# Performance work log

Hardware: AMD Instinct MI355X
Metric: run time of the kernel (lower is better)

Reference implementation:

```python
import jax, jax.numpy as jnp
import numpy as np

N, CIN, MID, OUT, H, W = 8, 512, 256, 256, 56, 56
HY, WY = 28, 28
EPS = 1e-5
K = 9  # 3x3 kernel points


def setup_inputs() -> dict:
    key = jax.random.key(0)
    ks = jax.random.split(key, 16)
    d = {}
    d["x"] = jax.random.normal(ks[0], (N, CIN, H, W), jnp.float32)
    d["y"] = jax.random.normal(ks[1], (N, MID, HY, WY), jnp.float32)
    d["conv1_w"] = jax.random.normal(ks[2], (MID, CIN), jnp.float32) * 0.02
    d["bn1_gamma"] = jax.random.uniform(ks[3], (MID,), jnp.float32) + 0.5
    d["bn1_beta"] = jax.random.normal(ks[4], (MID,), jnp.float32) * 0.1
    d["bn1_mean"] = jax.random.normal(ks[5], (MID,), jnp.float32) * 0.1
    d["bn1_var"] = jax.random.uniform(ks[6], (MID,), jnp.float32) + 0.5
    d["att_w"] = jax.random.normal(ks[7], (2, 2 * MID), jnp.float32) * 0.02
    d["att_b"] = jax.random.normal(ks[8], (2,), jnp.float32) * 0.1
    d["off_w"] = jax.random.normal(ks[9], (2 * K, MID, 3, 3), jnp.float32) * 0.01
    d["dcn_w"] = jax.random.normal(ks[10], (OUT, MID, 3, 3), jnp.float32) * 0.02
    d["bn2_gamma"] = jax.random.uniform(ks[11], (OUT,), jnp.float32) + 0.5
    d["bn2_beta"] = jax.random.normal(ks[12], (OUT,), jnp.float32) * 0.1
    d["bn2_mean"] = jax.random.normal(ks[13], (OUT,), jnp.float32) * 0.1
    d["bn2_var"] = jax.random.uniform(ks[14], (OUT,), jnp.float32) + 0.5
    return d


def _bn(v, gamma, beta, mean, var):
    # eval-mode BatchNorm2d
    scale = gamma * jax.lax.rsqrt(var + EPS)
    return v * scale[None, :, None, None] + (beta - mean * scale)[None, :, None, None]


def _conv3x3(x, w):
    return jax.lax.conv_general_dilated(
        x, w, window_strides=(1, 1), padding=((1, 1), (1, 1)),
        dimension_numbers=("NCHW", "OIHW", "NCHW"))


def _bilinear_sample(img, sy, sx):
    # img: [C,H,W]; sy,sx: [K,H,W] float sample coords; zero padding outside.
    Hc, Wc = img.shape[1], img.shape[2]
    y0 = jnp.floor(sy)
    x0 = jnp.floor(sx)
    wy1 = sy - y0
    wx1 = sx - x0

    def gather(yi, xi):
        valid = (yi >= 0) & (yi <= Hc - 1) & (xi >= 0) & (xi <= Wc - 1)
        yc = jnp.clip(yi, 0, Hc - 1).astype(jnp.int32)
        xc = jnp.clip(xi, 0, Wc - 1).astype(jnp.int32)
        return img[:, yc, xc] * valid[None].astype(img.dtype)  # [C,K,H,W]

    out = (gather(y0, x0) * ((1 - wy1) * (1 - wx1))[None]
           + gather(y0, x0 + 1) * ((1 - wy1) * wx1)[None]
           + gather(y0 + 1, x0) * (wy1 * (1 - wx1))[None]
           + gather(y0 + 1, x0 + 1) * (wy1 * wx1)[None])
    return out  # [C,K,H,W]


def _deform_conv(x, offset, weight):
    # x:[N,C,H,W]; offset:[N,2K,H,W] (per kernel point: dy then dx);
    # weight:[O,C,3,3]; stride 1, pad 1 -> same spatial shape.
    n, c, h, w = x.shape
    off = offset.reshape(n, K, 2, h, w)
    ky, kx = jnp.meshgrid(jnp.arange(3), jnp.arange(3), indexing="ij")
    ky = ky.reshape(K).astype(x.dtype)
    kx = kx.reshape(K).astype(x.dtype)
    gy = jnp.arange(h, dtype=x.dtype)
    gx = jnp.arange(w, dtype=x.dtype)
    base_y = gy[None, :, None] - 1.0 + ky[:, None, None]  # [K,H,1]
    base_x = gx[None, None, :] - 1.0 + kx[:, None, None]  # [K,1,W]
    sy = base_y[None] + off[:, :, 0]  # [N,K,H,W]
    sx = base_x[None] + off[:, :, 1]
    sampled = jax.vmap(_bilinear_sample)(x, sy, sx)  # [N,C,K,H,W]
    return jnp.einsum("nckhw,ock->nohw", sampled, weight.reshape(weight.shape[0], c, K))


def _cf_forward(x, y, conv1_w, bn1_gamma, bn1_beta, bn1_mean, bn1_var,
                att_w, att_b, off_w, dcn_w, bn2_gamma, bn2_beta, bn2_mean, bn2_var):
    n, _, h, w = x.shape
    # conv1: 1x1 conv + BN
    xm = jnp.einsum("nchw,mc->nmhw", x, conv1_w)
    xm = _bn(xm, bn1_gamma, bn1_beta, bn1_mean, bn1_var)
    # nearest-upsample y to (h, w)  (torch F.interpolate nearest)
    iy = (jnp.arange(h) * y.shape[2]) // h
    ix = (jnp.arange(w) * y.shape[3]) // w
    yu = y[:, :, iy][:, :, :, ix]
    # attention fuse: cat -> 1x1 conv -> sigmoid -> weighted sum
    z = jnp.concatenate([xm, yu], axis=1)
    z = jnp.einsum("nchw,oc->nohw", z, att_w) + att_b[None, :, None, None]
    z = jax.nn.sigmoid(z)
    xf = xm * z[:, 0:1] + yu * z[:, 1:2]
    # LIC: offset-predicting 3x3 conv, then deformable 3x3 conv, then BN
    off = _conv3x3(xf, off_w)
    out = _deform_conv(xf, off, dcn_w)
    out = _bn(out, bn2_gamma, bn2_beta, bn2_mean, bn2_var)
    return out, xf


def reference(x, y, conv1_w, bn1_gamma, bn1_beta, bn1_mean, bn1_var,
              att_w, att_b, off_w, dcn_w, bn2_gamma, bn2_beta, bn2_mean, bn2_var):
    return _cf_forward(x, y, conv1_w, bn1_gamma, bn1_beta, bn1_mean, bn1_var,
                       att_w, att_b, off_w, dcn_w, bn2_gamma, bn2_beta, bn2_mean, bn2_var)
```

## Files before the change

kernel.cpp:

```cpp
#include <hip/hip_runtime.h>
#include <math.h>

#define N_   8
#define CIN  512
#define MID  256
#define OUTC 256
#define H_   56
#define W_   56
#define HW   3136
#define EPS  1e-5f

typedef __attribute__((ext_vector_type(8))) short short8;
typedef __attribute__((ext_vector_type(4))) float floatx4;

__device__ __forceinline__ float bf2f(unsigned short b) {
  unsigned int u = ((unsigned int)b) << 16;
  return __builtin_bit_cast(float, u);
}
__device__ __forceinline__ unsigned short f2bf(float f) {
  unsigned int u = __builtin_bit_cast(unsigned int, f);
  unsigned int r = u + 0x7fffu + ((u >> 16) & 1u);
  return (unsigned short)(r >> 16);
}
__device__ __forceinline__ unsigned int pack2bf(float f0, float f1) {
  unsigned int u0 = __builtin_bit_cast(unsigned int, f0);
  unsigned int u1 = __builtin_bit_cast(unsigned int, f1);
  u0 += 0x7fffu + ((u0 >> 16) & 1u);
  u1 += 0x7fffu + ((u1 >> 16) & 1u);
  return (u0 >> 16) | (u1 & 0xffff0000u);
}

#define XF_BF_BYTES  (N_*HW*MID*2)
#define OFF_BYTES    (N_*HW*18*4)
#define WBF_BYTES    (256*2304*2)
#define WK2_BYTES    (2*72*64*8*2)
#define W1_BYTES     (64*256*8*2)
#define XB_BYTES     ((size_t)N_*HW*CIN*2)

__global__ __launch_bounds__(256) void prep_wbf(const float* __restrict__ dcn_w,
                                                unsigned short* __restrict__ wbf) {
  int e = blockIdx.x * 256 + threadIdx.x;
  int rb  = e >> 11;
  int rem = e & 2047;
  int o   = rem >> 3;
  int j   = e & 7;
  int r   = rb * 8 + j;
  int tap = r >> 8;
  int c   = r & 255;
  wbf[e] = f2bf(dcn_w[(o * 256 + c) * 9 + tap]);
}

__global__ __launch_bounds__(256) void prep_wk2(const float* __restrict__ off_w,
                                                unsigned short* __restrict__ wk2) {
  int e = blockIdx.x * 256 + threadIdx.x;
  int j  = e & 7;
  int l  = (e >> 3) & 63;
  int q  = e >> 9;
  int ot = (q >= 72) ? 1 : 0;
  int ks = q - ot * 72;
  int o  = ot * 16 + (l & 15);
  int r  = ks * 32 + ((l >> 4) << 3) + j;
  int tap = r >> 8;
  int c   = r & 255;
  float v = (o < 18) ? off_w[(o * 256 + c) * 9 + tap] : 0.f;
  wk2[e] = f2bf(v);
}

__global__ __launch_bounds__(256) void prep_w1(const float* __restrict__ conv1_w,
                                               unsigned short* __restrict__ w1bf) {
  int e = blockIdx.x * 256 + threadIdx.x;
  int rb = e >> 11;
  int m  = (e >> 3) & 255;
  int j  = e & 7;
  int c  = rb * 8 + j;
  w1bf[e] = f2bf(conv1_w[m * 512 + c]);
}

#define TP 72
__global__ __launch_bounds__(256) void prep_x(const float* __restrict__ x,
                                              unsigned short* __restrict__ xb) {
  __shared__ unsigned short T[32 * TP];
  const int t  = threadIdx.x;
  const int n  = blockIdx.z;
  const int c0 = blockIdx.y * 32;
  const int p0 = blockIdx.x * 64;

  {
    int c = t >> 3, pg = t & 7;
    const float4* src = (const float4*)(x + ((size_t)(n * CIN + c0 + c)) * HW + p0 + pg * 8);
    float4 v0 = src[0];
    float4 v1 = src[1];
    unsigned int d0 = pack2bf(v0.x, v0.y), d1 = pack2bf(v0.z, v0.w);
    unsigned int d2 = pack2bf(v1.x, v1.y), d3 = pack2bf(v1.z, v1.w);
    uint2 a; a.x = d0; a.y = d1;
    uint2 b; b.x = d2; b.y = d3;
    *(uint2*)&T[c * TP + pg * 8]     = a;
    *(uint2*)&T[c * TP + pg * 8 + 4] = b;
  }
  __syncthreads();
  {
    int p = t >> 2, cq = t & 3;
    unsigned short o8[8];
    #pragma unroll
    for (int j = 0; j < 8; ++j) o8[j] = T[(cq * 8 + j) * TP + p];
    *(short8*)(xb + ((size_t)(n * HW) + p0 + p) * CIN + c0 + cq * 8) = *(short8*)o8;
  }
}

#define K1SP 520
#define XSP  264

__global__ __launch_bounds__(256) void k1_gemm(
    const unsigned short* __restrict__ xb,
    const unsigned short* __restrict__ w1bf,
    const float* __restrict__ y,
    const float* __restrict__ g1, const float* __restrict__ b1,
    const float* __restrict__ m1, const float* __restrict__ v1,
    const float* __restrict__ att_w, const float* __restrict__ att_b,
    float* __restrict__ xf_out,
    unsigned short* __restrict__ xf_bf) {
  __shared__ unsigned short S[32 * K1SP];
  __shared__ float part[2][32][17];
  __shared__ float zz[2][32];

  const int t    = threadIdx.x;
  const int n    = blockIdx.x / 98;
  const int pix0 = (blockIdx.x % 98) * 32;

  {
    const int p = t >> 3, cg = t & 7;
    const short8* src = (const short8*)(xb + ((size_t)(n * HW) + pix0 + p) * CIN) + cg * 8;
    short8* dst = (short8*)&S[p * K1SP + cg * 64];
    #pragma unroll
    for (int j = 0; j < 8; ++j) dst[j] = src[j];
  }
  __syncthreads();

  const int w  = t >> 6;
  const int l  = t & 63;
  const int lo = l & 15;
  const int hi = l >> 4;

  floatx4 acc[4][2];
  #pragma unroll
  for (int i = 0; i < 4; ++i)
    #pragma unroll
    for (int j = 0; j < 2; ++j)
      acc[i][j] = (floatx4){0.f, 0.f, 0.f, 0.f};

  const short8* wbase = (const short8*)w1bf;

  #pragma unroll 4
  for (int ks = 0; ks < 16; ++ks) {
    int rb = ks * 4 + hi;
    const short8* wp = wbase + ((rb << 8) + (w << 6) + lo);
    short8 wa0 = wp[0];
    short8 wa1 = wp[16];
    short8 wa2 = wp[32];
    short8 wa3 = wp[48];
    const unsigned short* sp = &S[lo * K1SP + (ks << 5) + (hi << 3)];
    short8 sb0 = *(const short8*)sp;
    short8 sb1 = *(const short8*)(sp + 16 * K1SP);
    acc[0][0] = __builtin_amdgcn_mfma_f32_16x16x32_bf16(wa0, sb0, acc[0][0], 0, 0, 0);
    acc[0][1] = __builtin_amdgcn_mfma_f32_16x16x32_bf16(wa0, sb1, acc[0][1], 0, 0, 0);
    acc[1][0] = __builtin_amdgcn_mfma_f32_16x16x32_bf16(wa1, sb0, acc[1][0], 0, 0, 0);
    acc[1][1] = __builtin_amdgcn_mfma_f32_16x16x32_bf16(wa1, sb1, acc[1][1], 0, 0, 0);
    acc[2][0] = __builtin_amdgcn_mfma_f32_16x16x32_bf16(wa2, sb0, acc[2][0], 0, 0, 0);
    acc[2][1] = __builtin_amdgcn_mfma_f32_16x16x32_bf16(wa2, sb1, acc[2][1], 0, 0, 0);
    acc[3][0] = __builtin_amdgcn_mfma_f32_16x16x32_bf16(wa3, sb0, acc[3][0], 0, 0, 0);
    acc[3][1] = __builtin_amdgcn_mfma_f32_16x16x32_bf16(wa3, sb1, acc[3][1], 0, 0, 0);
  }

  const int pixA = pix0 + lo, pixB = pixA + 16;
  const int hA = pixA / 56, wxA = pixA - hA * 56;
  const int hB = pixB / 56, wxB = pixB - hB * 56;
  const int yoA = (hA >> 1) * 28 + (wxA >> 1);
  const int yoB = (hB >> 1) * 28 + (wxB >> 1);
  const float* yb = y + (size_t)n * MID * 784;

  float xmv[4][2][4];
  float s0A = 0.f, s0B = 0.f, s1A = 0.f, s1B = 0.f;
  #pragma unroll
  for (int i = 0; i < 4; ++i) {
    #pragma unroll
    for (int r = 0; r < 4; ++r) {
      int o = (w << 6) + (i << 4) + (hi << 2) + r;
      float sc = g1[o] * rsqrtf(v1[o] + EPS);
      float sh = fmaf(-m1[o], sc, b1[o]);
      float xA = fmaf(acc[i][0][r], sc, sh);
      float xB = fmaf(acc[i][1][r], sc, sh);
      xmv[i][0][r] = xA; xmv[i][1][r] = xB;
      float yA = yb[o * 784 + yoA];
      float yB = yb[o * 784 + yoB];
      float a0x = att_w[o], a0y = att_w[256 + o];
      float a1x = att_w[512 + o], a1y = att_w[768 + o];
      s0A = fmaf(a0x, xA, fmaf(a0y, yA, s0A));
      s0B = fmaf(a0x, xB, fmaf(a0y, yB, s0B));
      s1A = fmaf(a1x, xA, fmaf(a1y, yA, s1A));
      s1B = fmaf(a1x, xB, fmaf(a1y, yB, s1B));
    }
  }
  {
    int slot = (w << 2) + hi;
    part[0][lo][slot]      = s0A;
    part[0][16 + lo][slot] = s0B;
    part[1][lo][slot]      = s1A;
    part[1][16 + lo][slot] = s1B;
  }
  __syncthreads();
  if (t < 64) {
    int a = t >> 5, pp = t & 31;
    float s = att_b[a];
    #pragma unroll
    for (int g = 0; g < 16; ++g) s += part[a][pp][g];
    zz[a][pp] = 1.f / (1.f + expf(-s));
  }
  __syncthreads();

  {
    unsigned short* Sx = S;
    float z0A = zz[0][lo], z0B = zz[0][16 + lo];
    float z1A = zz[1][lo], z1B = zz[1][16 + lo];
    #pragma unroll
    for (int i = 0; i < 4; ++i) {
      #pragma unroll
      for (int r = 0; r < 4; ++r) {
        int o = (w << 6) + (i << 4) + (hi << 2) + r;
        float yA = yb[o * 784 + yoA];
        float yB = yb[o * 784 + yoB];
        float xfA = fmaf(xmv[i][0][r], z0A, yA * z1A);
        float xfB = fmaf(xmv[i][1][r], z0B, yB * z1B);
        float* ob = xf_out + (size_t)(n * MID + o) * HW;
        ob[pixA] = xfA;
        ob[pixB] = xfB;
        Sx[lo * XSP + o]        = f2bf(xfA);
        Sx[(16 + lo) * XSP + o] = f2bf(xfB);
      }
    }
  }
  __syncthreads();
  {
    const unsigned short* Sx = S;
    const int p = t >> 3, cg = t & 7;
    unsigned short* dst = xf_bf + ((size_t)(n * HW) + pix0 + p) * MID + cg * 32;
    #pragma unroll
    for (int j = 0; j < 4; ++j)
      *(short8*)(dst + j * 8) = *(const short8*)&Sx[p * XSP + cg * 32 + j * 8];
  }
}

#define K2P  32
#define K2SP 264

__global__ __launch_bounds__(256) void k2_offconv_mfma(
    const unsigned short* __restrict__ xf_bf,
    const unsigned short* __restrict__ wk2,
    float* __restrict__ off_out) {
  __shared__ unsigned short S[K2P * K2SP];
  __shared__ float red2[2][K2P][19];

  const int t    = threadIdx.x;
  const int n    = blockIdx.x / 98;
  const int pix0 = (blockIdx.x % 98) * K2P;

  const int l  = t & 63;
  const int lo = l & 15;
  const int hi = l >> 4;
  const int w  = t >> 6;
  const int pt = w & 1;
  const int kh = w >> 1;

  floatx4 acc0 = {0.f, 0.f, 0.f, 0.f};
  floatx4 acc1 = {0.f, 0.f, 0.f, 0.f};

  const int p   = t >> 3;
  const int cg  = t & 7;
  const int pix = pix0 + p;
  const int hh  = pix / 56;
  const int ww  = pix - hh * 56;

  const short8* wb8 = (const short8*)wk2;

  for (int tap = 0; tap < 9; ++tap) {
    const int ky = tap / 3, kx = tap - (tap / 3) * 3;
    const int yy = hh - 1 + ky, xx = ww - 1 + kx;
    const bool valid = ((unsigned)yy < 56u) && ((unsigned)xx < 56u);
    const int src = ((n * HW) + yy * 56 + xx) << 8;

    __syncthreads();
    #pragma unroll
    for (int g = 0; g < 4; ++g) {
      const int c0 = g * 64 + cg * 8;
      short8 v = (short8){0,0,0,0,0,0,0,0};
      if (valid) v = *(const short8*)(xf_bf + src + c0);
      *(short8*)&S[p * K2SP + c0] = v;
    }
    __syncthreads();

    #pragma unroll
    for (int s = 0; s < 4; ++s) {
      const int kst = kh * 4 + s;
      const int ks  = tap * 8 + kst;
      short8 bfrag = *(const short8*)&S[(pt * 16 + lo) * K2SP + kst * 32 + hi * 8];
      short8 a0 = wb8[(0 * 72 + ks) * 64 + l];
      short8 a1 = wb8[(1 * 72 + ks) * 64 + l];
      acc0 = __builtin_amdgcn_mfma_f32_16x16x32_bf16(a0, bfrag, acc0, 0, 0, 0);
      acc1 = __builtin_amdgcn_mfma_f32_16x16x32_bf16(a1, bfrag, acc1, 0, 0, 0);
    }
  }

  #pragma unroll
  for (int r = 0; r < 4; ++r) {
    int row = hi * 4 + r;
    red2[kh][pt * 16 + lo][row] = acc0[r];
    int o1 = 16 + row;
    if (o1 < 18) red2[kh][pt * 16 + lo][o1] = acc1[r];
  }
  __syncthreads();
  for (int e = t; e < K2P * 18; e += 256) {
    int pp = e / 18, oo = e - pp * 18;
    float sres = red2[0][pp][oo] + red2[1][pp][oo];
    off_out[((size_t)(n * HW) + pix0) * 18 + e] = sres;
  }
}

#define PB 32
#define SPITCH 264

__global__ __launch_bounds__(256) void k3_deform_mfma(
    const unsigned short* __restrict__ xf_bf, const float* __restrict__ off_in,
    const unsigned short* __restrict__ wbf,
    const float* __restrict__ g2, const float* __restrict__ b2,
    const float* __restrict__ m2, const float* __restrict__ v2,
    float* __restrict__ out) {
  __shared__ unsigned short S[PB * SPITCH];
  __shared__ float cw[288][4];
  __shared__ int   ad[288][4];
  __shared__ float offs[PB * 18];

  const int t    = threadIdx.x;
  const int n    = blockIdx.x / 98;
  const int pix0 = (blockIdx.x % 98) * PB;

  for (int e = t; e < PB * 18; e += 256)
    offs[e] = off_in[((size_t)(n * HW) + pix0) * 18 + e];
  __syncthreads();

  for (int e = t; e < 288; e += 256) {
    int p = e / 9, k = e - p * 9;
    int ky = k / 3, kx = k - ky * 3;
    int pix = pix0 + p;
    int hh = pix / 56, ww = pix - hh * 56;
    float sy = (float)(hh - 1 + ky) + offs[p * 18 + 2 * k];
    float sx = (float)(ww - 1 + kx) + offs[p * 18 + 2 * k + 1];
    float y0f = floorf(sy), x0f = floorf(sx);
    int y0 = (int)y0f, x0 = (int)x0f;
    float wy = sy - y0f, wx = sx - x0f;
    float w00 = (1.f - wy) * (1.f - wx), w01 = (1.f - wy) * wx;
    float w10 = wy * (1.f - wx),         w11 = wy * wx;
    bool yv0 = (unsigned)y0 < 56u, yv1 = (unsigned)(y0 + 1) < 56u;
    bool xv0 = (unsigned)x0 < 56u, xv1 = (unsigned)(x0 + 1) < 56u;
    int base = n * HW;
    ad[e][0] = (yv0 && xv0) ? (base + y0 * 56 + x0) * 256         : 0;
    ad[e][1] = (yv0 && xv1) ? (base + y0 * 56 + x0 + 1) * 256     : 0;
    ad[e][2] = (yv1 && xv0) ? (base + (y0+1) * 56 + x0) * 256     : 0;
    ad[e][3] = (yv1 && xv1) ? (base + (y0+1) * 56 + x0 + 1) * 256 : 0;
    cw[e][0] = (yv0 && xv0) ? w00 : 0.f;
    cw[e][1] = (yv0 && xv1) ? w01 : 0.f;
    cw[e][2] = (yv1 && xv0) ? w10 : 0.f;
    cw[e][3] = (yv1 && xv1) ? w11 : 0.f;
  }

  const int w  = t >> 6;
  const int l  = t & 63;
  const int lo = l & 15;
  const int hi = l >> 4;

  floatx4 acc[4][2];
  #pragma unroll
  for (int i = 0; i < 4; ++i)
    #pragma unroll
    for (int j = 0; j < 2; ++j)
      acc[i][j] = (floatx4){0.f, 0.f, 0.f, 0.f};

  const short8* wbase = (const short8*)wbf;

  const int sp_p  = t >> 3;
  const int sp_cg = t & 7;

  for (int tap = 0; tap < 9; ++tap) {
    __syncthreads();
    {
      const int s = sp_p * 9 + tap;
      const int a0 = ad[s][0], a1 = ad[s][1], a2 = ad[s][2], a3 = ad[s][3];
      const float w0 = cw[s][0], w1 = cw[s][1], w2 = cw[s][2], w3 = cw[s][3];
      #pragma unroll
      for (int g = 0; g < 4; ++g) {
        const int c0 = g * 64 + sp_cg * 8;
        short8 va = *(const short8*)(xf_bf + a0 + c0);
        short8 vb = *(const short8*)(xf_bf + a1 + c0);
        short8 vc = *(const short8*)(xf_bf + a2 + c0);
        short8 vd = *(const short8*)(xf_bf + a3 + c0);
        unsigned int pk[4];
        #pragma unroll
        for (int u = 0; u < 4; ++u) {
          float f0 = w0 * bf2f((unsigned short)va[2*u]);
          f0 = fmaf(w1, bf2f((unsigned short)vb[2*u]), f0);
          f0 = fmaf(w2, bf2f((unsigned short)vc[2*u]), f0);
          f0 = fmaf(w3, bf2f((unsigned short)vd[2*u]), f0);
          float f1 = w0 * bf2f((unsigned short)va[2*u+1]);
          f1 = fmaf(w1, bf2f((unsigned short)vb[2*u+1]), f1);
          f1 = fmaf(w2, bf2f((unsigned short)vc[2*u+1]), f1);
          f1 = fmaf(w3, bf2f((unsigned short)vd[2*u+1]), f1);
          pk[u] = pack2bf(f0, f1);
        }
        uint4 ov; ov.x = pk[0]; ov.y = pk[1]; ov.z = pk[2]; ov.w = pk[3];
        *(uint4*)&S[sp_p * SPITCH + c0] = ov;
      }
    }
    __syncthreads();

    #pragma unroll
    for (int ks = 0; ks < 8; ++ks) {
      int rb = tap * 32 + ks * 4 + hi;
      const short8* wp = wbase + ((rb << 8) + (w << 6) + lo);
      short8 wa0 = wp[0];
      short8 wa1 = wp[16];
      short8 wa2 = wp[32];
      short8 wa3 = wp[48];
      const unsigned short* sp = &S[lo * SPITCH + (ks << 5) + (hi << 3)];
      short8 sb0 = *(const short8*)sp;
      short8 sb1 = *(const short8*)(sp + 16 * SPITCH);
      acc[0][0] = __builtin_amdgcn_mfma_f32_16x16x32_bf16(wa0, sb0, acc[0][0], 0, 0, 0);
      acc[0][1] = __builtin_amdgcn_mfma_f32_16x16x32_bf16(wa0, sb1, acc[0][1], 0, 0, 0);
      acc[1][0] = __builtin_amdgcn_mfma_f32_16x16x32_bf16(wa1, sb0, acc[1][0], 0, 0, 0);
      acc[1][1] = __builtin_amdgcn_mfma_f32_16x16x32_bf16(wa1, sb1, acc[1][1], 0, 0, 0);
      acc[2][0] = __builtin_amdgcn_mfma_f32_16x16x32_bf16(wa2, sb0, acc[2][0], 0, 0, 0);
      acc[2][1] = __builtin_amdgcn_mfma_f32_16x16x32_bf16(wa2, sb1, acc[2][1], 0, 0, 0);
      acc[3][0] = __builtin_amdgcn_mfma_f32_16x16x32_bf16(wa3, sb0, acc[3][0], 0, 0, 0);
      acc[3][1] = __builtin_amdgcn_mfma_f32_16x16x32_bf16(wa3, sb1, acc[3][1], 0, 0, 0);
    }
  }

  #pragma unroll
  for (int i = 0; i < 4; ++i) {
    #pragma unroll
    for (int r = 0; r < 4; ++r) {
      int o = (w << 6) + (i << 4) + (hi << 2) + r;
      float scv = g2[o] * rsqrtf(v2[o] + EPS);
      float shv = b2[o] - m2[o] * scv;
      float* ob = out + ((size_t)(n * OUTC + o)) * HW + pix0;
      ob[lo]      = fmaf(acc[i][0][r], scv, shv);
      ob[16 + lo] = fmaf(acc[i][1][r], scv, shv);
    }
  }
}

extern "C" void kernel_launch(void* const* d_in, const int* in_sizes, int n_in,
                              void* d_out, int out_size, void* d_ws, size_t ws_size,
                              hipStream_t stream) {
  const float* x       = (const float*)d_in[0];
  const float* y       = (const float*)d_in[1];
  const float* conv1_w = (const float*)d_in[2];
  const float* g1      = (const float*)d_in[3];
  const float* b1      = (const float*)d_in[4];
  const float* m1      = (const float*)d_in[5];
  const float* v1      = (const float*)d_in[6];
  const float* att_w   = (const float*)d_in[7];
  const float* att_b   = (const float*)d_in[8];
  const float* off_w   = (const float*)d_in[9];
  const float* dcn_w   = (const float*)d_in[10];
  const float* g2      = (const float*)d_in[11];
  const float* b2      = (const float*)d_in[12];
  const float* m2      = (const float*)d_in[13];
  const float* v2      = (const float*)d_in[14];

  float* out    = (float*)d_out;
  float* xf_out = out + (size_t)N_ * OUTC * HW;

  char* ws = (char*)d_ws;
  unsigned short* xf_bf   = (unsigned short*)ws;
  float*          off_buf = (float*)(ws + XF_BF_BYTES);
  unsigned short* wbf     = (unsigned short*)(ws + XF_BF_BYTES + OFF_BYTES);
  unsigned short* wk2     = (unsigned short*)(ws + XF_BF_BYTES + OFF_BYTES + WBF_BYTES);
  unsigned short* w1bf    = (unsigned short*)(ws + XF_BF_BYTES + OFF_BYTES + WBF_BYTES + WK2_BYTES);
  unsigned short* xb      = (unsigned short*)(ws + XF_BF_BYTES + OFF_BYTES + WBF_BYTES + WK2_BYTES + W1_BYTES);

  hipLaunchKernelGGL(prep_wbf, dim3(2304), dim3(256), 0, stream, dcn_w, wbf);
  hipLaunchKernelGGL(prep_wk2, dim3(288), dim3(256), 0, stream, off_w, wk2);
  hipLaunchKernelGGL(prep_w1, dim3(512), dim3(256), 0, stream, conv1_w, w1bf);
  hipLaunchKernelGGL(prep_x, dim3(49, 16, N_), dim3(256), 0, stream, x, xb);
  hipLaunchKernelGGL(k1_gemm, dim3(784), dim3(256), 0, stream,
                     xb, w1bf, y, g1, b1, m1, v1, att_w, att_b, xf_out, xf_bf);
  hipLaunchKernelGGL(k2_offconv_mfma, dim3(784), dim3(256), 0, stream,
                     xf_bf, wk2, off_buf);
  hipLaunchKernelGGL(k3_deform_mfma, dim3(784), dim3(256), 0, stream,
                     xf_bf, off_buf, wbf, g2, b2, m2, v2, out);
}
```

Baseline: 299.6 us.

## Software-pipeline deform gather with double-buffered LDS and rework offset conv split

The deformable conv kernel now issues the bilinear gathers for the next tap into registers before the MFMA loop of the current tap, then blends them into a second LDS buffer, so global-load latency overlaps matrix math. The blend uses packed float2 math, and launch bounds request three blocks per SM. The offset conv uses 16-pixel blocks with each wave taking a K-slice, which doubles the grid and needs a 4-way reduction. Block indexing is interleaved across batch images in all three kernels. The prefetch holds 64 extra VGPRs of uint4 data, which risks register pressure or spills under the 3-block occupancy bound.

```diff
diff --git a/kernel.cpp b/kernel.cpp
--- a/kernel.cpp
+++ b/kernel.cpp
@@ -12,6 +12,7 @@
 
 typedef __attribute__((ext_vector_type(8))) short short8;
 typedef __attribute__((ext_vector_type(4))) float floatx4;
+typedef __attribute__((ext_vector_type(2))) float floatx2;
 
 __device__ __forceinline__ float bf2f(unsigned short b) {
   unsigned int u = ((unsigned int)b) << 16;
@@ -29,13 +30,18 @@
   u1 += 0x7fffu + ((u1 >> 16) & 1u);
   return (u0 >> 16) | (u1 & 0xffff0000u);
 }
+__device__ __forceinline__ floatx2 up2(unsigned int u) {
+  floatx2 r;
+  r.x = __builtin_bit_cast(float, u << 16);
+  r.y = __builtin_bit_cast(float, u & 0xffff0000u);
+  return r;
+}
 
 #define XF_BF_BYTES  (N_*HW*MID*2)
 #define OFF_BYTES    (N_*HW*18*4)
 #define WBF_BYTES    (256*2304*2)
 #define WK2_BYTES    (2*72*64*8*2)
 #define W1_BYTES     (64*256*8*2)
-#define XB_BYTES     ((size_t)N_*HW*CIN*2)
 
 __global__ __launch_bounds__(256) void prep_wbf(const float* __restrict__ dcn_w,
                                                 unsigned short* __restrict__ wbf) {
@@ -124,8 +130,8 @@
   __shared__ float zz[2][32];
 
   const int t    = threadIdx.x;
-  const int n    = blockIdx.x / 98;
-  const int pix0 = (blockIdx.x % 98) * 32;
+  const int n    = blockIdx.x & 7;
+  const int pix0 = (blockIdx.x >> 3) * 32;
 
   {
     const int p = t >> 3, cg = t & 7;
@@ -249,7 +255,7 @@
   }
 }
 
-#define K2P  32
+#define K2P  16
 #define K2SP 264
 
 __global__ __launch_bounds__(256) void k2_offconv_mfma(
@@ -257,24 +263,22 @@
     const unsigned short* __restrict__ wk2,
     float* __restrict__ off_out) {
   __shared__ unsigned short S[K2P * K2SP];
-  __shared__ float red2[2][K2P][19];
+  __shared__ float red2[4][K2P][19];
 
   const int t    = threadIdx.x;
-  const int n    = blockIdx.x / 98;
-  const int pix0 = (blockIdx.x % 98) * K2P;
+  const int n    = blockIdx.x & 7;
+  const int pix0 = (blockIdx.x >> 3) * K2P;
 
   const int l  = t & 63;
   const int lo = l & 15;
   const int hi = l >> 4;
   const int w  = t >> 6;
-  const int pt = w & 1;
-  const int kh = w >> 1;
 
   floatx4 acc0 = {0.f, 0.f, 0.f, 0.f};
   floatx4 acc1 = {0.f, 0.f, 0.f, 0.f};
 
-  const int p   = t >> 3;
-  const int cg  = t & 7;
+  const int p   = t >> 4;
+  const int cg  = t & 15;
   const int pix = pix0 + p;
   const int hh  = pix / 56;
   const int ww  = pix - hh * 56;
@@ -288,20 +292,24 @@
     const int src = ((n * HW) + yy * 56 + xx) << 8;
 
     __syncthreads();
-    #pragma unroll
-    for (int g = 0; g < 4; ++g) {
-      const int c0 = g * 64 + cg * 8;
-      short8 v = (short8){0,0,0,0,0,0,0,0};
-      if (valid) v = *(const short8*)(xf_bf + src + c0);
-      *(short8*)&S[p * K2SP + c0] = v;
+    {
+      const int c0 = cg * 16;
+      short8 v0 = (short8){0,0,0,0,0,0,0,0};
+      short8 v1 = v0;
+      if (valid) {
+        v0 = *(const short8*)(xf_bf + src + c0);
+        v1 = *(const short8*)(xf_bf + src + c0 + 8);
+      }
+      *(short8*)&S[p * K2SP + c0]     = v0;
+      *(short8*)&S[p * K2SP + c0 + 8] = v1;
     }
     __syncthreads();
 
     #pragma unroll
-    for (int s = 0; s < 4; ++s) {
-      const int kst = kh * 4 + s;
+    for (int s = 0; s < 2; ++s) {
+      const int kst = (w << 1) + s;
       const int ks  = tap * 8 + kst;
-      short8 bfrag = *(const short8*)&S[(pt * 16 + lo) * K2SP + kst * 32 + hi * 8];
+      short8 bfrag = *(const short8*)&S[lo * K2SP + kst * 32 + hi * 8];
       short8 a0 = wb8[(0 * 72 + ks) * 64 + l];
       short8 a1 = wb8[(1 * 72 + ks) * 64 + l];
       acc0 = __builtin_amdgcn_mfma_f32_16x16x32_bf16(a0, bfrag, acc0, 0, 0, 0);
@@ -312,14 +320,14 @@
   #pragma unroll
   for (int r = 0; r < 4; ++r) {
     int row = hi * 4 + r;
-    red2[kh][pt * 16 + lo][row] = acc0[r];
+    red2[w][lo][row] = acc0[r];
     int o1 = 16 + row;
-    if (o1 < 18) red2[kh][pt * 16 + lo][o1] = acc1[r];
+    if (o1 < 18) red2[w][lo][o1] = acc1[r];
   }
   __syncthreads();
   for (int e = t; e < K2P * 18; e += 256) {
     int pp = e / 18, oo = e - pp * 18;
-    float sres = red2[0][pp][oo] + red2[1][pp][oo];
+    float sres = red2[0][pp][oo] + red2[1][pp][oo] + red2[2][pp][oo] + red2[3][pp][oo];
     off_out[((size_t)(n * HW) + pix0) * 18 + e] = sres;
   }
 }
@@ -327,20 +335,20 @@
 #define PB 32
 #define SPITCH 264
 
-__global__ __launch_bounds__(256) void k3_deform_mfma(
+__global__ __launch_bounds__(256, 3) void k3_deform_mfma(
     const unsigned short* __restrict__ xf_bf, const float* __restrict__ off_in,
     const unsigned short* __restrict__ wbf,
     const float* __restrict__ g2, const float* __restrict__ b2,
     const float* __restrict__ m2, const float* __restrict__ v2,
     float* __restrict__ out) {
-  __shared__ unsigned short S[PB * SPITCH];
+  __shared__ unsigned short S[2][PB * SPITCH];
   __shared__ float cw[288][4];
   __shared__ int   ad[288][4];
   __shared__ float offs[PB * 18];
 
   const int t    = threadIdx.x;
-  const int n    = blockIdx.x / 98;
-  const int pix0 = (blockIdx.x % 98) * PB;
+  const int n    = blockIdx.x & 7;
+  const int pix0 = (blockIdx.x >> 3) * PB;
 
   for (int e = t; e < PB * 18; e += 256)
     offs[e] = off_in[((size_t)(n * HW) + pix0) * 18 + e];
@@ -370,6 +378,7 @@
     cw[e][2] = (yv1 && xv0) ? w10 : 0.f;
     cw[e][3] = (yv1 && xv1) ? w11 : 0.f;
   }
+  __syncthreads();
 
   const int w  = t >> 6;
   const int l  = t & 63;
@@ -388,38 +397,58 @@
   const int sp_p  = t >> 3;
   const int sp_cg = t & 7;
 
+  uint4 ld[4][4];
+
+  #define GATHER(tap_, dst_)                                            \
+    {                                                                   \
+      const int s_ = sp_p * 9 + (tap_);                                 \
+      const int a0_ = ad[s_][0], a1_ = ad[s_][1];                       \
+      const int a2_ = ad[s_][2], a3_ = ad[s_][3];                       \
+      _Pragma("unroll")                                                 \
+      for (int g_ = 0; g_ < 4; ++g_) {                                  \
+        const int c0_ = g_ * 64 + sp_cg * 8;                            \
+        dst_[0][g_] = *(const uint4*)(xf_bf + a0_ + c0_);               \
+        dst_[1][g_] = *(const uint4*)(xf_bf + a1_ + c0_);               \
+        dst_[2][g_] = *(const uint4*)(xf_bf + a2_ + c0_);               \
+        dst_[3][g_] = *(const uint4*)(xf_bf + a3_ + c0_);               \
+      }                                                                 \
+    }
+
+  #define BLEND(tap_, src_, buf_)                                       \
+    {                                                                   \
+      const int s_ = sp_p * 9 + (tap_);                                 \
+      const float w0_ = cw[s_][0], w1_ = cw[s_][1];                     \
+      const float w2_ = cw[s_][2], w3_ = cw[s_][3];                     \
+      _Pragma("unroll")                                                 \
+      for (int g_ = 0; g_ < 4; ++g_) {                                  \
+        const int c0_ = g_ * 64 + sp_cg * 8;                            \
+        unsigned int pk_[4];                                            \
+        const unsigned int* pa_ = (const unsigned int*)&src_[0][g_];    \
+        const unsigned int* pb_ = (const unsigned int*)&src_[1][g_];    \
+        const unsigned int* pc_ = (const unsigned int*)&src_[2][g_];    \
+        const unsigned int* pd_ = (const unsigned int*)&src_[3][g_];    \
+        _Pragma("unroll")                                               \
+        for (int u_ = 0; u_ < 4; ++u_) {                                \
+          floatx2 fa_ = up2(pa_[u_]), fb_ = up2(pb_[u_]);               \
+          floatx2 fc_ = up2(pc_[u_]), fd_ = up2(pd_[u_]);               \
+          floatx2 rr_ = fa_ * w0_ + fb_ * w1_ + fc_ * w2_ + fd_ * w3_;  \
+          pk_[u_] = pack2bf(rr_.x, rr_.y);                              \
+        }                                                               \
+        uint4 ov_; ov_.x = pk_[0]; ov_.y = pk_[1];                      \
+        ov_.z = pk_[2]; ov_.w = pk_[3];                                 \
+        *(uint4*)&S[buf_][sp_p * SPITCH + c0_] = ov_;                   \
+      }                                                                 \
+    }
+
+  GATHER(0, ld);
+  BLEND(0, ld, 0);
+
   for (int tap = 0; tap < 9; ++tap) {
+    uint4 ldn[4][4];
+    if (tap < 8) GATHER(tap + 1, ldn);
     __syncthreads();
-    {
-      const int s = sp_p * 9 + tap;
-      const int a0 = ad[s][0], a1 = ad[s][1], a2 = ad[s][2], a3 = ad[s][3];
-      const float w0 = cw[s][0], w1 = cw[s][1], w2 = cw[s][2], w3 = cw[s][3];
-      #pragma unroll
-      for (int g = 0; g < 4; ++g) {
-        const int c0 = g * 64 + sp_cg * 8;
-        short8 va = *(const short8*)(xf_bf + a0 + c0);
-        short8 vb = *(const short8*)(xf_bf + a1 + c0);
-        short8 vc = *(const short8*)(xf_bf + a2 + c0);
-        short8 vd = *(const short8*)(xf_bf + a3 + c0);
-        unsigned int pk[4];
-        #pragma unroll
-        for (int u = 0; u < 4; ++u) {
-          float f0 = w0 * bf2f((unsigned short)va[2*u]);
-          f0 = fmaf(w1, bf2f((unsigned short)vb[2*u]), f0);
-          f0 = fmaf(w2, bf2f((unsigned short)vc[2*u]), f0);
-          f0 = fmaf(w3, bf2f((unsigned short)vd[2*u]), f0);
-          float f1 = w0 * bf2f((unsigned short)va[2*u+1]);
-          f1 = fmaf(w1, bf2f((unsigned short)vb[2*u+1]), f1);
-          f1 = fmaf(w2, bf2f((unsigned short)vc[2*u+1]), f1);
-          f1 = fmaf(w3, bf2f((unsigned short)vd[2*u+1]), f1);
-          pk[u] = pack2bf(f0, f1);
-        }
-        uint4 ov; ov.x = pk[0]; ov.y = pk[1]; ov.z = pk[2]; ov.w = pk[3];
-        *(uint4*)&S[sp_p * SPITCH + c0] = ov;
-      }
-    }
-    __syncthreads();
-
+
+    const unsigned short* Sb = S[tap & 1];
     #pragma unroll
     for (int ks = 0; ks < 8; ++ks) {
       int rb = tap * 32 + ks * 4 + hi;
@@ -428,7 +457,7 @@
       short8 wa1 = wp[16];
       short8 wa2 = wp[32];
       short8 wa3 = wp[48];
-      const unsigned short* sp = &S[lo * SPITCH + (ks << 5) + (hi << 3)];
+      const unsigned short* sp = &Sb[lo * SPITCH + (ks << 5) + (hi << 3)];
       short8 sb0 = *(const short8*)sp;
       short8 sb1 = *(const short8*)(sp + 16 * SPITCH);
       acc[0][0] = __builtin_amdgcn_mfma_f32_16x16x32_bf16(wa0, sb0, acc[0][0], 0, 0, 0);
@@ -440,6 +469,8 @@
       acc[3][0] = __builtin_amdgcn_mfma_f32_16x16x32_bf16(wa3, sb0, acc[3][0], 0, 0, 0);
       acc[3][1] = __builtin_amdgcn_mfma_f32_16x16x32_bf16(wa3, sb1, acc[3][1], 0, 0, 0);
     }
+
+    if (tap < 8) BLEND(tap + 1, ldn, (tap + 1) & 1);
   }
 
   #pragma unroll
@@ -454,6 +485,8 @@
       ob[16 + lo] = fmaf(acc[i][1][r], scv, shv);
     }
   }
+  #undef GATHER
+  #undef BLEND
 }
 
 extern "C" void kernel_launch(void* const* d_in, const int* in_sizes, int n_in,
@@ -492,7 +525,7 @@
   hipLaunchKernelGGL(prep_x, dim3(49, 16, N_), dim3(256), 0, stream, x, xb);
   hipLaunchKernelGGL(k1_gemm, dim3(784), dim3(256), 0, stream,
                      xb, w1bf, y, g1, b1, m1, v1, att_w, att_b, xf_out, xf_bf);
-  hipLaunchKernelGGL(k2_offconv_mfma, dim3(784), dim3(256), 0, stream,
+  hipLaunchKernelGGL(k2_offconv_mfma, dim3(1568), dim3(256), 0, stream,
                      xf_bf, wk2, off_buf);
   hipLaunchKernelGGL(k3_deform_mfma, dim3(784), dim3(256), 0, stream,
                      xf_bf, off_buf, wbf, g2, b2, m2, v2, out);
```

New measurement: 271.5 us. 1.1x faster.
